# Performance work log

Hardware: AMD Instinct MI355X
Metric: run time of the kernel (lower is better)

The kernel has to match this reference:

```python
import jax, jax.numpy as jnp
import numpy as np
from jax import lax

B_SZ, SEQ, D_MODEL, D_STATE, DT_RANK = 4, 4096, 256, 16, 16


def setup_inputs() -> dict:
    key = jax.random.key(0)
    ks = jax.random.split(key, 12)
    d, n, r = D_MODEL, D_STATE, DT_RANK
    inp = {}
    inp["hidden_states"] = jax.random.normal(ks[0], (B_SZ, SEQ, d), jnp.float32)
    inp["in_proj_w"] = jax.random.normal(ks[1], (3 * d, d), jnp.float32) * (d ** -0.5)
    inp["x_proj_w"] = jax.random.normal(ks[2], (r + 2 * n, d), jnp.float32) * (d ** -0.5)
    s = r ** -0.5
    inp["dt_proj_w"] = jax.random.uniform(ks[3], (d, r), jnp.float32, -s, s)
    dt = jnp.exp(jax.random.uniform(ks[4], (d,), jnp.float32) * (np.log(0.1) - np.log(1e-3)) + np.log(1e-3))
    inp["dt_proj_b"] = dt + jnp.log(-jnp.expm1(-dt))  # inverse-softplus init
    inp["A_log"] = jnp.log(jnp.broadcast_to(jnp.arange(1, n + 1, dtype=jnp.float32), (d, n)))
    inp["D"] = jnp.ones((d,), jnp.float32)
    inp["out_proj1_w"] = jax.random.normal(ks[5], (d, d), jnp.float32) * (d ** -0.5)
    inp["conv_x_w"] = jax.random.normal(ks[6], (d, 1, 1), jnp.float32)
    inp["conv_x_b"] = jax.random.normal(ks[7], (d,), jnp.float32) * 0.1
    inp["conv_y_w"] = jax.random.normal(ks[8], (d, 1, 3), jnp.float32) * (3 ** -0.5)
    inp["conv_y_b"] = jax.random.normal(ks[9], (d,), jnp.float32) * 0.1
    inp["conv_z_w"] = jax.random.normal(ks[10], (d, 1, 5), jnp.float32) * (5 ** -0.5)
    inp["conv_z_b"] = jax.random.normal(ks[11], (d,), jnp.float32) * 0.1
    return inp


def _silu(x):
    return x * jax.nn.sigmoid(x)


def _dwconv(x, w, b):
    # x: (b, d, l); w: (d, 1, k) depthwise; 'same' padding (odd k)
    k = w.shape[-1]
    pad = (k - 1) // 2
    out = lax.conv_general_dilated(
        x, w, window_strides=(1,), padding=[(pad, pad)],
        dimension_numbers=("NCH", "OIH", "NCH"), feature_group_count=x.shape[1])
    return out + b[None, :, None]


def _selective_scan(u, delta, A, B, C, D, delta_bias):
    # u, delta: (b,d,l); A: (d,n); B,C: (b,n,l); D, delta_bias: (d,)
    delta = jax.nn.softplus(delta + delta_bias[None, :, None])
    dA = jnp.exp(jnp.einsum("bdl,dn->lbdn", delta, A))          # (l,b,d,n)
    dBu = jnp.einsum("bdl,bnl,bdl->lbdn", delta, B, u)           # (l,b,d,n)
    Ct = jnp.transpose(C, (2, 0, 1))                             # (l,b,n)

    def step(h, inp):
        dA_t, dBu_t, C_t = inp
        h = dA_t * h + dBu_t                                     # (b,d,n)
        y = jnp.einsum("bdn,bn->bd", h, C_t)
        return h, y

    h0 = jnp.zeros(u.shape[:2] + (A.shape[1],), u.dtype)
    _, ys = lax.scan(step, h0, (dA, dBu, Ct))                    # ys: (l,b,d)
    y = jnp.transpose(ys, (1, 2, 0))                             # (b,d,l)
    return y + D[None, :, None] * u


def reference(hidden_states, in_proj_w, x_proj_w, dt_proj_w, dt_proj_b, A_log, D,
              out_proj1_w, conv_x_w, conv_x_b, conv_y_w, conv_y_b, conv_z_w, conv_z_b):
    b, l, d = hidden_states.shape
    xyz = jnp.einsum("ble,de->bdl", hidden_states, in_proj_w)    # (b, 3d, l)
    x, y, z = jnp.split(xyz, 3, axis=1)                          # each (b,d,l)
    A = -jnp.exp(A_log.astype(jnp.float32))
    x = _silu(_dwconv(x, conv_x_w, conv_x_b))
    y = _silu(_dwconv(y, conv_y_w, conv_y_b))
    z = _silu(_dwconv(z, conv_z_w, conv_z_b))
    x_dbl = jnp.einsum("bdl,ed->ble", x, x_proj_w)               # (b,l,r+2n)
    dt_r, Bm, Cm = jnp.split(x_dbl, [DT_RANK, DT_RANK + D_STATE], axis=-1)
    # dt_proj applies bias here; selective_scan adds delta_bias again (faithful to source)
    dt = jnp.einsum("blr,dr->bdl", dt_r, dt_proj_w) + dt_proj_b[None, :, None]
    Bm = jnp.transpose(Bm, (0, 2, 1))                            # (b,n,l)
    Cm = jnp.transpose(Cm, (0, 2, 1))
    p = _selective_scan(x, dt, A, Bm, Cm, D.astype(jnp.float32), dt_proj_b.astype(jnp.float32))
    p = jnp.transpose(p, (0, 2, 1))                              # (b,l,d)
    y = jnp.transpose(y, (0, 2, 1))
    z = jnp.transpose(z, (0, 2, 1))
    l1 = jnp.einsum("bld,ed->ble", p * y, out_proj1_w)
    l2 = l1 * z
    l2 = _dwconv(jnp.transpose(l2, (0, 2, 1)), conv_x_w, conv_x_b)
    return jnp.transpose(l2, (0, 2, 1))                          # (b,l,d)
```

## Files before the change

kernel.cpp:

```cpp
#include <hip/hip_runtime.h>
#include <hip/hip_bf16.h>
#include <math.h>

typedef __hip_bfloat16 bf16;
typedef __attribute__((ext_vector_type(8))) short bf16x8;
typedef __attribute__((ext_vector_type(4))) float f32x4;

#define B_SZ 4
#define SEQ  4096
#define DM   256
#define NST  16
#define NCHK 64
#define LC   (SEQ/NCHK)
#define MT   (B_SZ*SEQ)
#define CT   4

__device__ __forceinline__ float silu_f(float v){ return v / (1.f + __expf(-v)); }
__device__ __forceinline__ float softplus_f(float v){
  return (v > 15.f) ? v : __logf(1.f + __expf(v));
}
__device__ __forceinline__ short f2bf(float f){
  union { bf16 h; short s; } u; u.h = __float2bfloat16(f); return u.s;
}
__device__ __forceinline__ float bf2f(short s){
  union { unsigned int i; float f; } v;
  v.i = ((unsigned int)(unsigned short)s) << 16; return v.f;
}
__device__ __forceinline__ float4 bf4_to_f4(uint2 q){
  float4 f;
  f.x = bf2f((short)(q.x & 0xffffu)); f.y = bf2f((short)(q.x >> 16));
  f.z = bf2f((short)(q.y & 0xffffu)); f.w = bf2f((short)(q.y >> 16));
  return f;
}
__device__ __forceinline__ short4 f4_to_bf4(float4 f){
  short4 s; s.x = f2bf(f.x); s.y = f2bf(f.y); s.z = f2bf(f.z); s.w = f2bf(f.w);
  return s;
}

template<int CTRL>
__device__ __forceinline__ float dpp_add_step(float v){
  int x = __builtin_amdgcn_update_dpp(0, __float_as_int(v), CTRL, 0xf, 0xf, true);
  return v + __int_as_float(x);
}

template<int EPI, bool A2M, bool ABF, bool OBF>
__global__ __launch_bounds__(256)
void mfma_gemm_k(const void* __restrict__ Av, const void* __restrict__ A2v,
                 const float* __restrict__ Bw, void* __restrict__ Outv,
                 int N, int K,
                 const float* __restrict__ bias, const short* __restrict__ zc,
                 const float* __restrict__ cwx)
{
  constexpr int BM = 128, BN = 128, BK = 32, LDP = 40;
  __shared__ short As[BM * LDP];
  __shared__ short Bs[BN * LDP];
  const int tid  = threadIdx.x;
  const int wave = tid >> 6, lane = tid & 63;
  const int quad = lane >> 4, l16 = lane & 15;
  const int wm = (wave & 1) * 64, wn = (wave >> 1) * 64;
  const int m0 = blockIdx.y * BM, n0 = blockIdx.x * BN;
  const int srow = tid >> 3;
  const int skq  = (tid & 7) * 4;

  f32x4 acc[4][4] = {};

  for (int k0 = 0; k0 < K; k0 += BK) {
    #pragma unroll
    for (int p = 0; p < 4; p++) {
      int row = p * 32 + srow;
      size_t ga = (size_t)(m0 + row) * K + k0 + skq;
      float4 q;
      if constexpr (ABF) q = bf4_to_f4(*(const uint2*)((const short*)Av + ga));
      else               q = *(const float4*)((const float*)Av + ga);
      if constexpr (A2M) {
        float4 r = bf4_to_f4(*(const uint2*)((const short*)A2v + ga));
        q.x *= r.x; q.y *= r.y; q.z *= r.z; q.w *= r.w;
      }
      *(short4*)&As[row * LDP + skq] = f4_to_bf4(q);
      size_t gb = (size_t)(n0 + row) * K + k0 + skq;
      *(short4*)&Bs[row * LDP + skq] = f4_to_bf4(*(const float4*)(Bw + gb));
    }
    __syncthreads();
    bf16x8 fa[4], fb[4];
    #pragma unroll
    for (int i = 0; i < 4; i++) {
      fa[i] = *(const bf16x8*)&As[(wm + i * 16 + l16) * LDP + quad * 8];
      fb[i] = *(const bf16x8*)&Bs[(wn + i * 16 + l16) * LDP + quad * 8];
    }
    #pragma unroll
    for (int i = 0; i < 4; i++)
      #pragma unroll
      for (int j = 0; j < 4; j++)
        acc[i][j] = __builtin_amdgcn_mfma_f32_16x16x32_bf16(fa[i], fb[j], acc[i][j], 0, 0, 0);
    __syncthreads();
  }

  #pragma unroll
  for (int i = 0; i < 4; i++) {
    #pragma unroll
    for (int j = 0; j < 4; j++) {
      int n = n0 + wn + j * 16 + l16;
      #pragma unroll
      for (int r = 0; r < 4; r++) {
        int m = m0 + wm + i * 16 + quad * 4 + r;
        float v = acc[i][j][r];
        if constexpr (EPI == 2)
          v = v * bf2f(zc[(size_t)m * N + n]) * cwx[n] + bias[n];
        if constexpr (OBF) ((short*)Outv)[(size_t)m * N + n] = f2bf(v);
        else               ((float*)Outv)[(size_t)m * N + n] = v;
      }
    }
  }
}

template<int EPI, bool ABF>
__global__ __launch_bounds__(256)
void gemm_k(const void* __restrict__ Av,
            const float* __restrict__ Bw, void* __restrict__ Out,
            int M, int N, int K, int lda,
            const float* __restrict__ bias)
{
  constexpr int TM = 64, TN = 64, TK = 16;
  __shared__ __align__(16) float As[TK][TM + 4];
  __shared__ __align__(16) float Bs[TK][TN + 4];
  const int tid = threadIdx.x;
  const int tn = tid & 15, tm = tid >> 4;
  const int n0 = blockIdx.x * TN, m0 = blockIdx.y * TM;
  float acc[4][4] = {};
  const int ml = tid >> 2;
  const int kq = (tid & 3) << 2;

  for (int k0 = 0; k0 < K; k0 += TK) {
    {
      size_t off = (size_t)(m0 + ml) * lda + k0 + kq;
      float4 q;
      if constexpr (ABF) q = bf4_to_f4(*(const uint2*)((const short*)Av + off));
      else               q = *(const float4*)((const float*)Av + off);
      As[kq+0][ml] = q.x; As[kq+1][ml] = q.y; As[kq+2][ml] = q.z; As[kq+3][ml] = q.w;
    }
    {
      float v0 = 0.f, v1 = 0.f, v2 = 0.f, v3 = 0.f;
      if (n0 + ml < N) {
        float4 q = *(const float4*)(Bw + (size_t)(n0 + ml) * K + k0 + kq);
        v0 = q.x; v1 = q.y; v2 = q.z; v3 = q.w;
      }
      Bs[kq+0][ml] = v0; Bs[kq+1][ml] = v1; Bs[kq+2][ml] = v2; Bs[kq+3][ml] = v3;
    }
    __syncthreads();
    #pragma unroll
    for (int k = 0; k < TK; k++) {
      float4 av = *(const float4*)&As[k][tm << 2];
      float4 bv = *(const float4*)&Bs[k][tn << 2];
      float a[4] = {av.x, av.y, av.z, av.w};
      float b[4] = {bv.x, bv.y, bv.z, bv.w};
      #pragma unroll
      for (int i = 0; i < 4; i++)
        #pragma unroll
        for (int j = 0; j < 4; j++)
          acc[i][j] = fmaf(a[i], b[j], acc[i][j]);
    }
    __syncthreads();
  }

  #pragma unroll
  for (int i = 0; i < 4; i++) {
    int m = m0 + (tm << 2) + i;
    #pragma unroll
    for (int j = 0; j < 4; j++) {
      int n = n0 + (tn << 2) + j;
      if (n < N) {
        float v = acc[i][j];
        if constexpr (EPI == 0) {
          ((float*)Out)[(size_t)m * N + n] = v;
        } else {
          ((float*)Out)[(size_t)m * N + n] = softplus_f(v + 2.f * bias[n]);
        }
      }
    }
  }
}

__global__ __launch_bounds__(256)
void conv_silu_k(const short* __restrict__ xyzb,
                 const float* __restrict__ wx, const float* __restrict__ bx,
                 const float* __restrict__ wy, const float* __restrict__ by,
                 const float* __restrict__ wz, const float* __restrict__ bz,
                 short* __restrict__ xcb, short* __restrict__ ycb,
                 short* __restrict__ zcb)
{
  int idx = blockIdx.x * 256 + threadIdx.x;
  int c4 = idx % 192;
  int lt = idx / 192;
  int row0 = lt * CT;
  int l0 = row0 & (SEQ - 1);

  float4 win[CT + 4];
  #pragma unroll
  for (int i = 0; i < CT + 4; i++) {
    int l = l0 + i - 2;
    if (l >= 0 && l < SEQ)
      win[i] = bf4_to_f4(*(const uint2*)(xyzb + (size_t)(row0 + i - 2) * 768 + c4 * 4));
    else
      win[i] = make_float4(0.f, 0.f, 0.f, 0.f);
  }

  if (c4 < 64) {
    int d = c4 * 4;
    float4 w  = *(const float4*)&wx[d];
    float4 bb = *(const float4*)&bx[d];
    #pragma unroll
    for (int t = 0; t < CT; t++) {
      float4 v = win[t + 2], o;
      o.x = silu_f(fmaf(v.x, w.x, bb.x));
      o.y = silu_f(fmaf(v.y, w.y, bb.y));
      o.z = silu_f(fmaf(v.z, w.z, bb.z));
      o.w = silu_f(fmaf(v.w, w.w, bb.w));
      *(short4*)&xcb[(size_t)(row0 + t) * 256 + d] = f4_to_bf4(o);
    }
  } else if (c4 < 128) {
    int d = (c4 - 64) * 4;
    float wq[4][3];
    #pragma unroll
    for (int q = 0; q < 4; q++)
      #pragma unroll
      for (int j = 0; j < 3; j++) wq[q][j] = wy[(d + q) * 3 + j];
    float4 bb = *(const float4*)&by[d];
    #pragma unroll
    for (int t = 0; t < CT; t++) {
      float a0 = bb.x, a1 = bb.y, a2 = bb.z, a3 = bb.w;
      #pragma unroll
      for (int j = 0; j < 3; j++) {
        float4 v = win[t + 1 + j];
        a0 = fmaf(v.x, wq[0][j], a0);
        a1 = fmaf(v.y, wq[1][j], a1);
        a2 = fmaf(v.z, wq[2][j], a2);
        a3 = fmaf(v.w, wq[3][j], a3);
      }
      float4 o; o.x = silu_f(a0); o.y = silu_f(a1); o.z = silu_f(a2); o.w = silu_f(a3);
      *(short4*)&ycb[(size_t)(row0 + t) * 256 + d] = f4_to_bf4(o);
    }
  } else {
    int d = (c4 - 128) * 4;
    float wq[4][5];
    #pragma unroll
    for (int q = 0; q < 4; q++)
      #pragma unroll
      for (int j = 0; j < 5; j++) wq[q][j] = wz[(d + q) * 5 + j];
    float4 bb = *(const float4*)&bz[d];
    #pragma unroll
    for (int t = 0; t < CT; t++) {
      float a0 = bb.x, a1 = bb.y, a2 = bb.z, a3 = bb.w;
      #pragma unroll
      for (int j = 0; j < 5; j++) {
        float4 v = win[t + j];
        a0 = fmaf(v.x, wq[0][j], a0);
        a1 = fmaf(v.y, wq[1][j], a1);
        a2 = fmaf(v.z, wq[2][j], a2);
        a3 = fmaf(v.w, wq[3][j], a3);
      }
      float4 o; o.x = silu_f(a0); o.y = silu_f(a1); o.z = silu_f(a2); o.w = silu_f(a3);
      *(short4*)&zcb[(size_t)(row0 + t) * 256 + d] = f4_to_bf4(o);
    }
  }
}

template<bool PASSC>
__global__ __launch_bounds__(256)
void scan_k(const short* __restrict__ xcb,
            const float* __restrict__ dtv,
            const float* __restrict__ xdbl,
            const float* __restrict__ A_log,
            const float* __restrict__ Dp,
            const float* __restrict__ Hstart,
            float* __restrict__ Pbuf, float* __restrict__ hfbuf,
            short* __restrict__ poutb)
{
  __shared__ float2 du2_s[LC * 16];
  __shared__ float2 BC_s [PASSC ? LC * 16 : 16];
  __shared__ float  Bc_s [PASSC ? 16 : LC * 16];
  __shared__ float  y_s  [PASSC ? 16 * 65 : 16];
  const int tid = threadIdx.x;
  const int n = tid & 15, dl = tid >> 4;
  const int ch = blockIdx.x;
  const int d0 = blockIdx.y * 16;
  const int b  = blockIdx.z;
  const int d  = d0 + dl;
  const int t0 = ch * LC;
  const size_t brow = (size_t)b * SEQ;

  float u_r[4];
  #pragma unroll
  for (int i = 0; i < 4; i++) {
    int t = (tid >> 4) + i * 16;
    size_t row = brow + t0 + t;
    float uval = bf2f(xcb[row * 256 + d0 + n]);
    float dval = dtv[row * 256 + d0 + n];
    du2_s[t * 16 + n] = make_float2(dval, dval * uval);
    if constexpr (PASSC) {
      BC_s[t * 16 + n] = make_float2(xdbl[row * 48 + 16 + n],
                                     xdbl[row * 48 + 32 + n]);
      u_r[i] = uval;
    } else {
      Bc_s[t * 16 + n] = xdbl[row * 48 + 16 + n];
    }
  }
  __syncthreads();

  const float A_dn = -__expf(A_log[d * NST + n]);
  const size_t cidx = (((size_t)b * DM + d) * NST + n) * NCHK + ch;

  float h = PASSC ? Hstart[cidx] : 0.f;
  float P = 1.f;
  for (int t4 = 0; t4 < LC; t4 += 4) {
    float dA[4], dBu[4];
    #pragma unroll
    for (int j = 0; j < 4; j++) {
      float2 du = du2_s[(t4 + j) * 16 + dl];
      dA[j] = __expf(du.x * A_dn);
      if constexpr (PASSC) dBu[j] = du.y;
      else                 dBu[j] = du.y * Bc_s[(t4 + j) * 16 + n];
    }
    if constexpr (!PASSC) {
      #pragma unroll
      for (int j = 0; j < 4; j++) {
        h = fmaf(dA[j], h, dBu[j]);
        P *= dA[j];
      }
    } else {
      float yv[4];
      #pragma unroll
      for (int j = 0; j < 4; j++) {
        float2 bc = BC_s[(t4 + j) * 16 + n];
        h = fmaf(dA[j], h, dBu[j] * bc.x);
        yv[j] = h * bc.y;
      }
      #pragma unroll
      for (int j = 0; j < 4; j++) yv[j] = dpp_add_step<0x118>(yv[j]);
      #pragma unroll
      for (int j = 0; j < 4; j++) yv[j] = dpp_add_step<0x114>(yv[j]);
      #pragma unroll
      for (int j = 0; j < 4; j++) yv[j] = dpp_add_step<0x112>(yv[j]);
      #pragma unroll
      for (int j = 0; j < 4; j++) yv[j] = dpp_add_step<0x111>(yv[j]);
      if (n == 15)
        *(float4*)&y_s[dl * 65 + t4] = make_float4(yv[0], yv[1], yv[2], yv[3]);
    }
  }

  if constexpr (!PASSC) {
    Pbuf[cidx] = P;
    hfbuf[cidx] = h;
  } else {
    __syncthreads();
    const float Dval = Dp[d0 + n];
    #pragma unroll
    for (int i = 0; i < 4; i++) {
      int t = (tid >> 4) + i * 16;
      poutb[(brow + t0 + t) * 256 + d0 + n] =
          f2bf(fmaf(Dval, u_r[i], y_s[n * 65 + t]));
    }
  }
}

__global__ __launch_bounds__(256)
void scan_mid_k(const float* __restrict__ Pbuf, const float* __restrict__ hfbuf,
                float* __restrict__ Hstart)
{
  int tid = blockIdx.x * 256 + threadIdx.x;
  size_t base = (size_t)tid * NCHK;
  float H = 0.f;
  for (int c = 0; c < NCHK; c++) {
    Hstart[base + c] = H;
    H = Pbuf[base + c] * H + hfbuf[base + c];
  }
}

extern "C" void kernel_launch(void* const* d_in, const int* in_sizes, int n_in,
                              void* d_out, int out_size, void* d_ws, size_t ws_size,
                              hipStream_t stream)
{
  const float* hs    = (const float*)d_in[0];
  const float* w_in  = (const float*)d_in[1];
  const float* w_xp  = (const float*)d_in[2];
  const float* w_dt  = (const float*)d_in[3];
  const float* b_dt  = (const float*)d_in[4];
  const float* A_log = (const float*)d_in[5];
  const float* Dp    = (const float*)d_in[6];
  const float* w_o1  = (const float*)d_in[7];
  const float* cwx   = (const float*)d_in[8];
  const float* cbx   = (const float*)d_in[9];
  const float* cwy   = (const float*)d_in[10];
  const float* cby   = (const float*)d_in[11];
  const float* cwz   = (const float*)d_in[12];
  const float* cbz   = (const float*)d_in[13];

  char* wsb = (char*)d_ws;
  short* xyzb = (short*)wsb;
  short* xcb  = (short*)(wsb + (size_t)MT * 768 * 2);
  short* ycb  = xcb + (size_t)MT * 256;
  short* zcb  = ycb + (size_t)MT * 256;
  short* pbufb= zcb + (size_t)MT * 256;
  float* xdbl = (float*)(pbufb + (size_t)MT * 256);
  float* dtv  = xdbl + (size_t)MT * 48;
  float* Pb   = dtv  + (size_t)MT * 256;
  float* hf   = Pb   + (size_t)B_SZ * DM * NST * NCHK;
  float* Hs   = hf   + (size_t)B_SZ * DM * NST * NCHK;

  dim3 blk(256);

  mfma_gemm_k<0, false, false, true><<<dim3(768 / 128, MT / 128), blk, 0, stream>>>(
      hs, nullptr, w_in, xyzb, 768, 256, nullptr, nullptr, nullptr);

  conv_silu_k<<<dim3((MT / CT) * 192 / 256), blk, 0, stream>>>(
      xyzb, cwx, cbx, cwy, cby, cwz, cbz, xcb, ycb, zcb);

  gemm_k<0, true><<<dim3(1, MT / 64), blk, 0, stream>>>(
      xcb, w_xp, xdbl, MT, 48, 256, 256, nullptr);

  gemm_k<3, false><<<dim3(256 / 64, MT / 64), blk, 0, stream>>>(
      xdbl, w_dt, dtv, MT, 256, 16, 48, b_dt);

  scan_k<false><<<dim3(NCHK, DM / 16, B_SZ), blk, 0, stream>>>(
      xcb, dtv, xdbl, A_log, Dp, nullptr, Pb, hf, nullptr);
  scan_mid_k<<<dim3((B_SZ * DM * NST) / 256), blk, 0, stream>>>(Pb, hf, Hs);
  scan_k<true><<<dim3(NCHK, DM / 16, B_SZ), blk, 0, stream>>>(
      xcb, dtv, xdbl, A_log, Dp, Hs, nullptr, nullptr, pbufb);

  mfma_gemm_k<2, true, true, false><<<dim3(256 / 128, MT / 128), blk, 0, stream>>>(
      pbufb, ycb, w_o1, (float*)d_out, 256, 256, cbx, zcb, cwx);
}
```

Baseline: 225.8 us.

## Fuse x_proj and dt_proj GEMMs, transpose scan smem layout, swap GEMM grid axes

```diff
diff --git a/kernel.cpp b/kernel.cpp
--- a/kernel.cpp
+++ b/kernel.cpp
@@ -58,7 +58,7 @@
   const int wave = tid >> 6, lane = tid & 63;
   const int quad = lane >> 4, l16 = lane & 15;
   const int wm = (wave & 1) * 64, wn = (wave >> 1) * 64;
-  const int m0 = blockIdx.y * BM, n0 = blockIdx.x * BN;
+  const int m0 = blockIdx.x * BM, n0 = blockIdx.y * BN;
   const int srow = tid >> 3;
   const int skq  = (tid & 7) * 4;
 
@@ -113,35 +113,47 @@
   }
 }
 
-template<int EPI, bool ABF>
 __global__ __launch_bounds__(256)
-void gemm_k(const void* __restrict__ Av,
-            const float* __restrict__ Bw, void* __restrict__ Out,
-            int M, int N, int K, int lda,
-            const float* __restrict__ bias)
-{
-  constexpr int TM = 64, TN = 64, TK = 16;
+void gemm34_k(const short* __restrict__ xcb,
+              const float* __restrict__ Bw,
+              const float* __restrict__ wdt,
+              const float* __restrict__ bdt,
+              float* __restrict__ xdbl,
+              float* __restrict__ dtv)
+{
+  constexpr int TM = 64, TK = 16, NN = 48;
   __shared__ __align__(16) float As[TK][TM + 4];
-  __shared__ __align__(16) float Bs[TK][TN + 4];
+  __shared__ __align__(16) float Bs[TK][TM + 4];
+  __shared__ __align__(16) float dt_s[TM][20];
+  __shared__ __align__(16) float wdt_s[256][20];
   const int tid = threadIdx.x;
   const int tn = tid & 15, tm = tid >> 4;
-  const int n0 = blockIdx.x * TN, m0 = blockIdx.y * TM;
+  const int m0 = blockIdx.x * TM;
   float acc[4][4] = {};
   const int ml = tid >> 2;
   const int kq = (tid & 3) << 2;
 
-  for (int k0 = 0; k0 < K; k0 += TK) {
+  {
+    float4 q0 = *(const float4*)&wdt[tid * 16 + 0];
+    float4 q1 = *(const float4*)&wdt[tid * 16 + 4];
+    float4 q2 = *(const float4*)&wdt[tid * 16 + 8];
+    float4 q3 = *(const float4*)&wdt[tid * 16 + 12];
+    *(float4*)&wdt_s[tid][0]  = q0;
+    *(float4*)&wdt_s[tid][4]  = q1;
+    *(float4*)&wdt_s[tid][8]  = q2;
+    *(float4*)&wdt_s[tid][12] = q3;
+  }
+
+  for (int k0 = 0; k0 < 256; k0 += TK) {
     {
-      size_t off = (size_t)(m0 + ml) * lda + k0 + kq;
-      float4 q;
-      if constexpr (ABF) q = bf4_to_f4(*(const uint2*)((const short*)Av + off));
-      else               q = *(const float4*)((const float*)Av + off);
+      size_t off = (size_t)(m0 + ml) * 256 + k0 + kq;
+      float4 q = bf4_to_f4(*(const uint2*)(xcb + off));
       As[kq+0][ml] = q.x; As[kq+1][ml] = q.y; As[kq+2][ml] = q.z; As[kq+3][ml] = q.w;
     }
     {
       float v0 = 0.f, v1 = 0.f, v2 = 0.f, v3 = 0.f;
-      if (n0 + ml < N) {
-        float4 q = *(const float4*)(Bw + (size_t)(n0 + ml) * K + k0 + kq);
+      if (ml < NN) {
+        float4 q = *(const float4*)(Bw + (size_t)ml * 256 + k0 + kq);
         v0 = q.x; v1 = q.y; v2 = q.z; v3 = q.w;
       }
       Bs[kq+0][ml] = v0; Bs[kq+1][ml] = v1; Bs[kq+2][ml] = v2; Bs[kq+3][ml] = v3;
@@ -167,15 +179,42 @@
     int m = m0 + (tm << 2) + i;
     #pragma unroll
     for (int j = 0; j < 4; j++) {
-      int n = n0 + (tn << 2) + j;
-      if (n < N) {
-        float v = acc[i][j];
-        if constexpr (EPI == 0) {
-          ((float*)Out)[(size_t)m * N + n] = v;
-        } else {
-          ((float*)Out)[(size_t)m * N + n] = softplus_f(v + 2.f * bias[n]);
-        }
-      }
+      int n = (tn << 2) + j;
+      float v = acc[i][j];
+      if (n < NN) xdbl[(size_t)m * NN + n] = v;
+      if (tn < 4) dt_s[(tm << 2) + i][n] = v;
+    }
+  }
+  __syncthreads();
+
+  const int c0 = tid & 63, rg = tid >> 6;
+  float w[4][16];
+  float bb[4];
+  #pragma unroll
+  for (int cc = 0; cc < 4; cc++) {
+    int col = cc * 64 + c0;
+    #pragma unroll
+    for (int q = 0; q < 4; q++) {
+      float4 t = *(const float4*)&wdt_s[col][q * 4];
+      w[cc][q*4+0] = t.x; w[cc][q*4+1] = t.y; w[cc][q*4+2] = t.z; w[cc][q*4+3] = t.w;
+    }
+    bb[cc] = 2.f * bdt[col];
+  }
+  #pragma unroll
+  for (int rr = 0; rr < 16; rr++) {
+    int row = rg * 16 + rr;
+    float dr[16];
+    #pragma unroll
+    for (int q = 0; q < 4; q++) {
+      float4 t = *(const float4*)&dt_s[row][q * 4];
+      dr[q*4+0] = t.x; dr[q*4+1] = t.y; dr[q*4+2] = t.z; dr[q*4+3] = t.w;
+    }
+    #pragma unroll
+    for (int cc = 0; cc < 4; cc++) {
+      float s = bb[cc];
+      #pragma unroll
+      for (int k = 0; k < 16; k++) s = fmaf(dr[k], w[cc][k], s);
+      dtv[(size_t)(m0 + row) * 256 + cc * 64 + c0] = softplus_f(s);
     }
   }
 }
@@ -275,10 +314,10 @@
             float* __restrict__ Pbuf, float* __restrict__ hfbuf,
             short* __restrict__ poutb)
 {
-  __shared__ float2 du2_s[LC * 16];
-  __shared__ float2 BC_s [PASSC ? LC * 16 : 16];
-  __shared__ float  Bc_s [PASSC ? 16 : LC * 16];
-  __shared__ float  y_s  [PASSC ? 16 * 65 : 16];
+  __shared__ __align__(16) float2 du2_s[16 * 66];
+  __shared__ __align__(16) float2 BC_s [PASSC ? 16 * 66 : 2];
+  __shared__ __align__(16) float  Bc_s [PASSC ? 4 : 16 * 68];
+  __shared__ __align__(16) float  y_s  [PASSC ? 16 * 68 : 4];
   const int tid = threadIdx.x;
   const int n = tid & 15, dl = tid >> 4;
   const int ch = blockIdx.x;
@@ -292,16 +331,17 @@
   #pragma unroll
   for (int i = 0; i < 4; i++) {
     int t = (tid >> 4) + i * 16;
+    int dd = tid & 15;
     size_t row = brow + t0 + t;
-    float uval = bf2f(xcb[row * 256 + d0 + n]);
-    float dval = dtv[row * 256 + d0 + n];
-    du2_s[t * 16 + n] = make_float2(dval, dval * uval);
+    float uval = bf2f(xcb[row * 256 + d0 + dd]);
+    float dval = dtv[row * 256 + d0 + dd];
+    du2_s[dd * 66 + t] = make_float2(dval, dval * uval);
     if constexpr (PASSC) {
-      BC_s[t * 16 + n] = make_float2(xdbl[row * 48 + 16 + n],
-                                     xdbl[row * 48 + 32 + n]);
+      BC_s[dd * 66 + t] = make_float2(xdbl[row * 48 + 16 + dd],
+                                      xdbl[row * 48 + 32 + dd]);
       u_r[i] = uval;
     } else {
-      Bc_s[t * 16 + n] = xdbl[row * 48 + 16 + n];
+      Bc_s[dd * 68 + t] = xdbl[row * 48 + 16 + dd];
     }
   }
   __syncthreads();
@@ -312,27 +352,31 @@
   float h = PASSC ? Hstart[cidx] : 0.f;
   float P = 1.f;
   for (int t4 = 0; t4 < LC; t4 += 4) {
-    float dA[4], dBu[4];
-    #pragma unroll
-    for (int j = 0; j < 4; j++) {
-      float2 du = du2_s[(t4 + j) * 16 + dl];
-      dA[j] = __expf(du.x * A_dn);
-      if constexpr (PASSC) dBu[j] = du.y;
-      else                 dBu[j] = du.y * Bc_s[(t4 + j) * 16 + n];
-    }
+    float4 a = *(const float4*)&du2_s[dl * 66 + t4];
+    float4 c = *(const float4*)&du2_s[dl * 66 + t4 + 2];
+    float dA[4], du[4];
+    dA[0] = __expf(a.x * A_dn); du[0] = a.y;
+    dA[1] = __expf(a.z * A_dn); du[1] = a.w;
+    dA[2] = __expf(c.x * A_dn); du[2] = c.y;
+    dA[3] = __expf(c.z * A_dn); du[3] = c.w;
     if constexpr (!PASSC) {
+      float4 f = *(const float4*)&Bc_s[n * 68 + t4];
+      float Bv[4] = {f.x, f.y, f.z, f.w};
       #pragma unroll
       for (int j = 0; j < 4; j++) {
-        h = fmaf(dA[j], h, dBu[j]);
+        h = fmaf(dA[j], h, du[j] * Bv[j]);
         P *= dA[j];
       }
     } else {
+      float4 e = *(const float4*)&BC_s[n * 66 + t4];
+      float4 g = *(const float4*)&BC_s[n * 66 + t4 + 2];
+      float Bv[4] = {e.x, e.z, g.x, g.z};
+      float Cv[4] = {e.y, e.w, g.y, g.w};
       float yv[4];
       #pragma unroll
       for (int j = 0; j < 4; j++) {
-        float2 bc = BC_s[(t4 + j) * 16 + n];
-        h = fmaf(dA[j], h, dBu[j] * bc.x);
-        yv[j] = h * bc.y;
+        h = fmaf(dA[j], h, du[j] * Bv[j]);
+        yv[j] = h * Cv[j];
       }
       #pragma unroll
       for (int j = 0; j < 4; j++) yv[j] = dpp_add_step<0x118>(yv[j]);
@@ -343,7 +387,7 @@
       #pragma unroll
       for (int j = 0; j < 4; j++) yv[j] = dpp_add_step<0x111>(yv[j]);
       if (n == 15)
-        *(float4*)&y_s[dl * 65 + t4] = make_float4(yv[0], yv[1], yv[2], yv[3]);
+        *(float4*)&y_s[dl * 68 + t4] = make_float4(yv[0], yv[1], yv[2], yv[3]);
     }
   }
 
@@ -357,7 +401,7 @@
     for (int i = 0; i < 4; i++) {
       int t = (tid >> 4) + i * 16;
       poutb[(brow + t0 + t) * 256 + d0 + n] =
-          f2bf(fmaf(Dval, u_r[i], y_s[n * 65 + t]));
+          f2bf(fmaf(Dval, u_r[i], y_s[n * 68 + t]));
     }
   }
 }
@@ -408,17 +452,14 @@
 
   dim3 blk(256);
 
-  mfma_gemm_k<0, false, false, true><<<dim3(768 / 128, MT / 128), blk, 0, stream>>>(
+  mfma_gemm_k<0, false, false, true><<<dim3(MT / 128, 768 / 128), blk, 0, stream>>>(
       hs, nullptr, w_in, xyzb, 768, 256, nullptr, nullptr, nullptr);
 
   conv_silu_k<<<dim3((MT / CT) * 192 / 256), blk, 0, stream>>>(
       xyzb, cwx, cbx, cwy, cby, cwz, cbz, xcb, ycb, zcb);
 
-  gemm_k<0, true><<<dim3(1, MT / 64), blk, 0, stream>>>(
-      xcb, w_xp, xdbl, MT, 48, 256, 256, nullptr);
-
-  gemm_k<3, false><<<dim3(256 / 64, MT / 64), blk, 0, stream>>>(
-      xdbl, w_dt, dtv, MT, 256, 16, 48, b_dt);
+  gemm34_k<<<dim3(MT / 64), blk, 0, stream>>>(
+      xcb, w_xp, w_dt, b_dt, xdbl, dtv);
 
   scan_k<false><<<dim3(NCHK, DM / 16, B_SZ), blk, 0, stream>>>(
       xcb, dtv, xdbl, A_log, Dp, nullptr, Pb, hf, nullptr);
@@ -426,6 +467,6 @@
   scan_k<true><<<dim3(NCHK, DM / 16, B_SZ), blk, 0, stream>>>(
       xcb, dtv, xdbl, A_log, Dp, Hs, nullptr, nullptr, pbufb);
 
-  mfma_gemm_k<2, true, true, false><<<dim3(256 / 128, MT / 128), blk, 0, stream>>>(
+  mfma_gemm_k<2, true, true, false><<<dim3(MT / 128, 256 / 128), blk, 0, stream>>>(
       pbufb, ycb, w_o1, (float*)d_out, 256, 256, cbx, zcb, cwx);
 }
```

New measurement: 219.3 us. 2.9% less time.
